# Kernel optimization log

Measured on AMD Instinct MI355X. Metric: run time of the kernel, lower is better.

The kernel has to match this reference:

```python
import jax, jax.numpy as jnp
import numpy as np

B, L, H, NH, NB = 8, 200, 128, 4, 2
HD = H // NH
ITEM_NUM, TIME_SPAN = 50000, 256
PAD = -2.0**32 + 1.0


def setup_inputs() -> dict:
    key = jax.random.key(0)
    ks = jax.random.split(key, 32)
    def g(i, shape, s=0.02):
        return jax.random.normal(ks[i], shape, jnp.float32) * s
    item_emb = g(0, (ITEM_NUM + 1, H)).at[0].set(0.0)  # padding_idx=0
    return dict(
        user_ids=jax.random.randint(ks[1], (B,), 0, 1000),
        log_seqs=jax.random.randint(ks[2], (B, L), 0, ITEM_NUM),
        time_matrices=jax.random.randint(ks[3], (B, L, L), 0, TIME_SPAN + 1),
        pos_seqs=jax.random.randint(ks[4], (B, L), 0, ITEM_NUM + 1),
        neg_seqs=jax.random.randint(ks[5], (B, L), 0, ITEM_NUM + 1),
        item_emb=item_emb,
        pos_K_emb=g(6, (L, H)), pos_V_emb=g(7, (L, H)),
        time_K_emb=g(8, (TIME_SPAN + 1, H)), time_V_emb=g(9, (TIME_SPAN + 1, H)),
        attn_ln_g=jnp.ones((NB, H)), attn_ln_b=jnp.zeros((NB, H)),
        Wq=g(10, (NB, H, H)), bq=jnp.zeros((NB, H)),
        Wk=g(11, (NB, H, H)), bk=jnp.zeros((NB, H)),
        Wv=g(12, (NB, H, H)), bv=jnp.zeros((NB, H)),
        fwd_ln_g=jnp.ones((NB, H)), fwd_ln_b=jnp.zeros((NB, H)),
        W1=g(13, (NB, H, H)), b1=jnp.zeros((NB, H)),
        W2=g(14, (NB, H, H)), b2=jnp.zeros((NB, H)),
        last_ln_g=jnp.ones((H,)), last_ln_b=jnp.zeros((H,)),
    )


def _ln(x, g, b, eps=1e-8):
    m = x.mean(-1, keepdims=True)
    v = jnp.var(x, axis=-1, keepdims=True)
    return (x - m) / jnp.sqrt(v + eps) * g + b


def _heads(x):
    # [..., H] -> [NH, ..., HD]; matches torch.cat(torch.split(x, HD, -1), 0)
    y = x.reshape(x.shape[:-1] + (NH, HD))
    return jnp.moveaxis(y, -2, 0)


def reference(user_ids, log_seqs, time_matrices, pos_seqs, neg_seqs, item_emb,
              pos_K_emb, pos_V_emb, time_K_emb, time_V_emb,
              attn_ln_g, attn_ln_b, Wq, bq, Wk, bk, Wv, bv,
              fwd_ln_g, fwd_ln_b, W1, b1, W2, b2, last_ln_g, last_ln_b):
    # user_ids is unused in the original forward as well.
    tmask = log_seqs == 0                                  # [B,L] True = pad
    keep = (~tmask)[..., None].astype(jnp.float32)
    seqs = item_emb[log_seqs] * np.float32(np.sqrt(H))
    seqs = seqs * keep
    pKh = _heads(pos_K_emb)                                # [NH,L,HD]
    pVh = _heads(pos_V_emb)
    tKh = _heads(time_K_emb[time_matrices])                # [NH,B,L,L,HD]
    tVh = _heads(time_V_emb[time_matrices])
    causal = ~jnp.tril(jnp.ones((L, L), bool))             # True above diag -> masked
    bad = tmask[:, :, None] | causal[None]                 # [B,L,L]
    scale = np.float32(np.sqrt(HD))
    for i in range(NB):
        Qin = _ln(seqs, attn_ln_g[i], attn_ln_b[i])
        Qh = _heads(Qin @ Wq[i].T + bq[i])                 # [NH,B,L,HD]
        Kh = _heads(seqs @ Wk[i].T + bk[i])
        Vh = _heads(seqs @ Wv[i].T + bv[i])
        attn = (jnp.einsum('nbqd,nbkd->nbqk', Qh, Kh)
                + jnp.einsum('nbqd,nkd->nbqk', Qh, pKh)
                + jnp.einsum('nbqkd,nbqd->nbqk', tKh, Qh)) / scale
        attn = jnp.where(bad[None], PAD, attn)
        attn = jax.nn.softmax(attn, axis=-1)
        out = (jnp.einsum('nbqk,nbkd->nbqd', attn, Vh)
               + jnp.einsum('nbqk,nkd->nbqd', attn, pVh)
               + jnp.einsum('nbqk,nbqkd->nbqd', attn, tVh))
        out = jnp.moveaxis(out, 0, -2).reshape(seqs.shape)  # merge heads -> [B,L,H]
        seqs = Qin + out                                    # residual uses LN'd Q (as in source)
        seqs = _ln(seqs, fwd_ln_g[i], fwd_ln_b[i])
        ff = jax.nn.relu(seqs @ W1[i].T + b1[i]) @ W2[i].T + b2[i] + seqs
        seqs = ff * keep
    log_feats = _ln(seqs, last_ln_g, last_ln_b)
    pos_logits = (log_feats * item_emb[pos_seqs]).sum(-1)   # [B,L]
    neg_logits = (log_feats * item_emb[neg_seqs]).sum(-1)
    return pos_logits, neg_logits
```

## Files before the change

### kernel.cpp

```cpp
#include <hip/hip_runtime.h>

#define BB 8
#define LL 200
#define HH 128
#define NHEAD 4
#define HDIM 32
#define NBLK 2
#define BL (BB * LL)
#define NT 257
#define QT 8
#define NQT 25
#define SSP 208
#define KTP 66
#define TSP 132

static constexpr float SQRT_H    = 11.313708498984761f;
static constexpr float INV_SCALE = 0.17677669529663687f;
static constexpr float PADV      = -4294967295.0f;

__global__ void k_qkv_gemm(const float* __restrict__ seqs_in,
                           const int* __restrict__ log_seqs,
                           const float* __restrict__ item_emb,
                           const float* __restrict__ g, const float* __restrict__ bia,
                           const float* __restrict__ Wq, const float* __restrict__ bq,
                           const float* __restrict__ Wk, const float* __restrict__ bk,
                           const float* __restrict__ Wv, const float* __restrict__ bv,
                           const float* __restrict__ posK, const float* __restrict__ posV,
                           float* __restrict__ Qin, float* __restrict__ Q,
                           float* __restrict__ K, float* __restrict__ V) {
    int mt = blockIdx.x / 24, nt = blockIdx.x % 24;
    int matsel = nt >> 3;
    int jb = (nt & 7) * 16;
    int row0 = mt * 32;
    int tid = threadIdx.x;
    __shared__ float As[32 * TSP];
    __shared__ float Bs[16 * TSP];

    {
        int r = tid >> 3, seg = tid & 7;
        int row = row0 + r;
        float4 vv[4];
        if (seqs_in) {
            #pragma unroll
            for (int i = 0; i < 4; i++)
                vv[i] = *(const float4*)(seqs_in + (size_t)row * HH + seg * 16 + i * 4);
        } else {
            int idx = log_seqs[row];
            if (idx == 0) {
                #pragma unroll
                for (int i = 0; i < 4; i++) vv[i] = make_float4(0.f, 0.f, 0.f, 0.f);
            } else {
                #pragma unroll
                for (int i = 0; i < 4; i++) {
                    float4 e = *(const float4*)(item_emb + (size_t)idx * HH + seg * 16 + i * 4);
                    vv[i] = make_float4(e.x * SQRT_H, e.y * SQRT_H, e.z * SQRT_H, e.w * SQRT_H);
                }
            }
        }
        if (matsel == 0) {
            float s = 0.f, s2 = 0.f;
            #pragma unroll
            for (int i = 0; i < 4; i++) {
                s  += vv[i].x + vv[i].y + vv[i].z + vv[i].w;
                s2 += vv[i].x * vv[i].x + vv[i].y * vv[i].y + vv[i].z * vv[i].z + vv[i].w * vv[i].w;
            }
            #pragma unroll
            for (int off = 1; off < 8; off <<= 1) {
                s  += __shfl_xor(s, off);
                s2 += __shfl_xor(s2, off);
            }
            float mean = s * (1.f / HH);
            float var  = s2 * (1.f / HH) - mean * mean;
            float inv  = 1.f / sqrtf(var + 1e-8f);
            #pragma unroll
            for (int i = 0; i < 4; i++) {
                int k = seg * 16 + i * 4;
                float4 g4 = *(const float4*)(g + k);
                float4 b4 = *(const float4*)(bia + k);
                float4 y;
                y.x = (vv[i].x - mean) * inv * g4.x + b4.x;
                y.y = (vv[i].y - mean) * inv * g4.y + b4.y;
                y.z = (vv[i].z - mean) * inv * g4.z + b4.z;
                y.w = (vv[i].w - mean) * inv * g4.w + b4.w;
                *(float4*)&As[r * TSP + k] = y;
                if (nt == 0) *(float4*)(Qin + (size_t)row * HH + k) = y;
            }
        } else {
            #pragma unroll
            for (int i = 0; i < 4; i++)
                *(float4*)&As[r * TSP + seg * 16 + i * 4] = vv[i];
        }
    }
    {
        const float* W = (matsel == 0) ? Wq : (matsel == 1) ? Wk : Wv;
        int j = tid >> 4, seg = tid & 15;
        float4 w  = *(const float4*)(W + (size_t)(jb + j) * HH + seg * 8);
        float4 w2 = *(const float4*)(W + (size_t)(jb + j) * HH + seg * 8 + 4);
        *(float4*)&Bs[j * TSP + seg * 8]     = w;
        *(float4*)&Bs[j * TSP + seg * 8 + 4] = w2;
    }
    __syncthreads();

    int m = tid >> 3, jg = tid & 7;
    float acc0 = 0.f, acc1 = 0.f;
    const float* ar  = &As[m * TSP];
    const float* b0r = &Bs[(jg * 2) * TSP];
    const float* b1r = &Bs[(jg * 2 + 1) * TSP];
    #pragma unroll 4
    for (int k4 = 0; k4 < 32; k4++) {
        float4 a  = *(const float4*)(ar + k4 * 4);
        float4 b0 = *(const float4*)(b0r + k4 * 4);
        float4 b1 = *(const float4*)(b1r + k4 * 4);
        acc0 += a.x * b0.x + a.y * b0.y + a.z * b0.z + a.w * b0.w;
        acc1 += a.x * b1.x + a.y * b1.y + a.z * b1.z + a.w * b1.w;
    }
    int row = row0 + m;
    int col = jb + jg * 2;
    int l = row % LL;
    if (matsel == 0) {
        float2 bb = *(const float2*)(bq + col);
        *(float2*)(Q + (size_t)row * HH + col) =
            make_float2((acc0 + bb.x) * INV_SCALE, (acc1 + bb.y) * INV_SCALE);
    } else if (matsel == 1) {
        float2 bb = *(const float2*)(bk + col);
        float2 pk = *(const float2*)(posK + (size_t)l * HH + col);
        *(float2*)(K + (size_t)row * HH + col) =
            make_float2(acc0 + bb.x + pk.x, acc1 + bb.y + pk.y);
    } else {
        float2 bb = *(const float2*)(bv + col);
        float2 pv = *(const float2*)(posV + (size_t)l * HH + col);
        *(float2*)(V + (size_t)row * HH + col) =
            make_float2(acc0 + bb.x + pv.x, acc1 + bb.y + pv.y);
    }
}

__global__ void k_attn(const float* __restrict__ Q, const float* __restrict__ K,
                       const float* __restrict__ V,
                       const float* __restrict__ timeK, const float* __restrict__ timeV,
                       const int* __restrict__ tm,
                       float* __restrict__ att) {
    int bn = blockIdx.x & 31;
    int b = bn >> 2, n = bn & 3;
    int qt = (NQT - 1) - (blockIdx.x >> 5);
    int q0 = qt * QT;
    int kmax = q0 + QT - 1;
    int tid = threadIdx.x;
    int wv = tid >> 6, ln = tid & 63;

    __shared__ float KstT[2][HDIM * KTP];
    __shared__ float DTW[QT * NT];
    __shared__ float Ssc[QT * SSP];
    __shared__ float Ost[QT * HDIM];
    __shared__ int   tmst[QT * LL];

    Ost[tid] = 0.f;
    #pragma unroll
    for (int qi = 0; qi < QT; qi++)
        if (tid < LL)
            tmst[qi * LL + tid] = tm[((size_t)(b * LL + q0 + qi)) * LL + tid];

    int k2 = tid & 31, qi_c = tid >> 5;
    int q = q0 + qi_c;

    float qreg[HDIM];
    {
        const float* qp = Q + ((size_t)(b * LL + q)) * HH + n * HDIM;
        #pragma unroll
        for (int i = 0; i < 8; i++) {
            float4 v = *(const float4*)(qp + i * 4);
            qreg[i * 4 + 0] = v.x; qreg[i * 4 + 1] = v.y;
            qreg[i * 4 + 2] = v.z; qreg[i * 4 + 3] = v.w;
        }
    }

    const int nchS = (kmax >> 6) + 1;
    const int ncht = 5 + nchS;

    auto stage = [&](int c, float* buf) {
        #pragma unroll
        for (int p = 0; p < 2; p++) {
            int idx = tid + p * 256;
            int r = idx >> 3, d4 = idx & 7;
            float4 w = make_float4(0.f, 0.f, 0.f, 0.f);
            if (c < 5) {
                int tau = c * 64 + r;
                if (tau < NT) w = *(const float4*)(timeK + (size_t)tau * HH + n * HDIM + d4 * 4);
            } else {
                int k = (c - 5) * 64 + r;
                if (k < LL) w = *(const float4*)(K + ((size_t)(b * LL + k)) * HH + n * HDIM + d4 * 4);
            }
            buf[(d4 * 4 + 0) * KTP + r] = w.x;
            buf[(d4 * 4 + 1) * KTP + r] = w.y;
            buf[(d4 * 4 + 2) * KTP + r] = w.z;
            buf[(d4 * 4 + 3) * KTP + r] = w.w;
        }
    };

    stage(0, KstT[0]);
    __syncthreads();
    for (int c = 0; c < ncht; c++) {
        if (c + 1 < ncht) stage(c + 1, KstT[(c + 1) & 1]);
        const float* buf = KstT[c & 1];
        float a0 = 0.f, a1 = 0.f;
        #pragma unroll 4
        for (int d = 0; d < HDIM; d++) {
            float qv = qreg[d];
            float2 kv = *(const float2*)&buf[d * KTP + k2 * 2];
            a0 += qv * kv.x; a1 += qv * kv.y;
        }
        if (c < 5) {
            int tau0 = c * 64 + k2 * 2;
            if (tau0 < NT)     DTW[qi_c * NT + tau0]     = a0;
            if (tau0 + 1 < NT) DTW[qi_c * NT + tau0 + 1] = a1;
        } else {
            int k0 = (c - 5) * 64 + k2 * 2;
            if (k0 <= kmax)     Ssc[qi_c * SSP + k0]     = a0;
            if (k0 + 1 <= kmax) Ssc[qi_c * SSP + k0 + 1] = a1;
        }
        __syncthreads();
    }

    for (int rr = 0; rr < 2; rr++) {
        int qi = wv + rr * 4;
        int qq = q0 + qi;
        float sv[4];
        float m = PADV;
        #pragma unroll
        for (int jj = 0; jj < 4; jj++) {
            int k = ln + 64 * jj;
            sv[jj] = (k <= qq) ? (Ssc[qi * SSP + k] + DTW[qi * NT + tmst[qi * LL + k]]) : PADV;
            m = fmaxf(m, sv[jj]);
        }
        for (int off = 32; off; off >>= 1) m = fmaxf(m, __shfl_xor(m, off));
        float sum = 0.f;
        #pragma unroll
        for (int jj = 0; jj < 4; jj++) {
            int k = ln + 64 * jj;
            sv[jj] = (k <= qq) ? __expf(sv[jj] - m) : 0.f;
            sum += sv[jj];
        }
        for (int off = 32; off; off >>= 1) sum += __shfl_xor(sum, off);
        float inv = 1.f / sum;
        #pragma unroll
        for (int jj = 0; jj < 4; jj++) {
            int k = ln + 64 * jj;
            if (k < SSP) Ssc[qi * SSP + k] = (k <= qq) ? sv[jj] * inv : 0.f;
        }
    }
    __syncthreads();

    int d = tid & 31, kg = tid >> 5;
    float acc[QT] = {0,0,0,0,0,0,0,0};
    const float* vb  = V + ((size_t)(b * LL)) * HH + n * HDIM + d;
    const float* tvb = timeV + n * HDIM + d;
    for (int k = kg; k <= kmax; k += 8) {
        float v = vb[(size_t)k * HH];
        #pragma unroll
        for (int qi = 0; qi < QT; qi++) {
            float p  = Ssc[qi * SSP + k];
            float tv = tvb[(size_t)tmst[qi * LL + k] * HH];
            acc[qi] += p * (v + tv);
        }
    }
    #pragma unroll
    for (int qi = 0; qi < QT; qi++) atomicAdd(&Ost[qi * HDIM + d], acc[qi]);
    __syncthreads();
    {
        int qi = tid >> 5;
        att[((size_t)(b * LL + q0 + qi)) * HH + n * HDIM + (tid & 31)] = Ost[tid];
    }
}

__global__ void k_ff1(const float* __restrict__ Qin, const float* __restrict__ att,
                      const float* __restrict__ g, const float* __restrict__ bia,
                      const float* __restrict__ W1, const float* __restrict__ b1,
                      float* __restrict__ h1) {
    int mt = blockIdx.x >> 3, jb = (blockIdx.x & 7) * 16;
    int row0 = mt * 16;
    int tid = threadIdx.x;
    __shared__ float As[16 * TSP];
    __shared__ float Bs[16 * TSP];

    {
        int r = tid >> 4, seg = tid & 15;
        int row = row0 + r;
        float4 vv[2];
        #pragma unroll
        for (int i = 0; i < 2; i++) {
            int k = seg * 8 + i * 4;
            float4 q4 = *(const float4*)(Qin + (size_t)row * HH + k);
            float4 a4 = *(const float4*)(att + (size_t)row * HH + k);
            vv[i] = make_float4(q4.x + a4.x, q4.y + a4.y, q4.z + a4.z, q4.w + a4.w);
        }
        float s = 0.f, s2 = 0.f;
        #pragma unroll
        for (int i = 0; i < 2; i++) {
            s  += vv[i].x + vv[i].y + vv[i].z + vv[i].w;
            s2 += vv[i].x * vv[i].x + vv[i].y * vv[i].y + vv[i].z * vv[i].z + vv[i].w * vv[i].w;
        }
        #pragma unroll
        for (int off = 1; off < 16; off <<= 1) {
            s  += __shfl_xor(s, off);
            s2 += __shfl_xor(s2, off);
        }
        float mean = s * (1.f / HH);
        float var  = s2 * (1.f / HH) - mean * mean;
        float inv  = 1.f / sqrtf(var + 1e-8f);
        #pragma unroll
        for (int i = 0; i < 2; i++) {
            int k = seg * 8 + i * 4;
            float4 g4 = *(const float4*)(g + k);
            float4 b4 = *(const float4*)(bia + k);
            float4 y;
            y.x = (vv[i].x - mean) * inv * g4.x + b4.x;
            y.y = (vv[i].y - mean) * inv * g4.y + b4.y;
            y.z = (vv[i].z - mean) * inv * g4.z + b4.z;
            y.w = (vv[i].w - mean) * inv * g4.w + b4.w;
            *(float4*)&As[r * TSP + k] = y;
        }
    }
    {
        int j = tid >> 4, seg = tid & 15;
        *(float4*)&Bs[j * TSP + seg * 8]     = *(const float4*)(W1 + (size_t)(jb + j) * HH + seg * 8);
        *(float4*)&Bs[j * TSP + seg * 8 + 4] = *(const float4*)(W1 + (size_t)(jb + j) * HH + seg * 8 + 4);
    }
    __syncthreads();

    int m = tid >> 4, j = tid & 15;
    float acc = 0.f;
    const float* ar = &As[m * TSP];
    const float* br = &Bs[j * TSP];
    #pragma unroll 4
    for (int k4 = 0; k4 < 32; k4++) {
        float4 a = *(const float4*)(ar + k4 * 4);
        float4 b = *(const float4*)(br + k4 * 4);
        acc += a.x * b.x + a.y * b.y + a.z * b.z + a.w * b.w;
    }
    int col = jb + j;
    float t = acc + b1[col];
    h1[(size_t)(row0 + m) * HH + col] = t > 0.f ? t : 0.f;
}

__global__ void k_ff2(const float* __restrict__ h1,
                      const float* __restrict__ Qin, const float* __restrict__ att,
                      const float* __restrict__ g, const float* __restrict__ bia,
                      const float* __restrict__ W2, const float* __restrict__ b2,
                      const int* __restrict__ log_seqs,
                      float* __restrict__ out) {
    int mt = blockIdx.x >> 3, jb = (blockIdx.x & 7) * 16;
    int row0 = mt * 16;
    int tid = threadIdx.x;
    __shared__ float As[16 * TSP];
    __shared__ float Bs[16 * TSP];
    __shared__ float mu[16], rstd[16];

    {
        int r = tid >> 4, seg = tid & 15;
        int row = row0 + r;
        #pragma unroll
        for (int i = 0; i < 2; i++) {
            int k = seg * 8 + i * 4;
            *(float4*)&As[r * TSP + k] = *(const float4*)(h1 + (size_t)row * HH + k);
        }
        float s = 0.f, s2 = 0.f;
        #pragma unroll
        for (int i = 0; i < 2; i++) {
            int k = seg * 8 + i * 4;
            float4 q4 = *(const float4*)(Qin + (size_t)row * HH + k);
            float4 a4 = *(const float4*)(att + (size_t)row * HH + k);
            float4 v = make_float4(q4.x + a4.x, q4.y + a4.y, q4.z + a4.z, q4.w + a4.w);
            s  += v.x + v.y + v.z + v.w;
            s2 += v.x * v.x + v.y * v.y + v.z * v.z + v.w * v.w;
        }
        #pragma unroll
        for (int off = 1; off < 16; off <<= 1) {
            s  += __shfl_xor(s, off);
            s2 += __shfl_xor(s2, off);
        }
        float mean = s * (1.f / HH);
        float var  = s2 * (1.f / HH) - mean * mean;
        if (seg == 0) { mu[r] = mean; rstd[r] = 1.f / sqrtf(var + 1e-8f); }
    }
    {
        int j = tid >> 4, seg = tid & 15;
        *(float4*)&Bs[j * TSP + seg * 8]     = *(const float4*)(W2 + (size_t)(jb + j) * HH + seg * 8);
        *(float4*)&Bs[j * TSP + seg * 8 + 4] = *(const float4*)(W2 + (size_t)(jb + j) * HH + seg * 8 + 4);
    }
    __syncthreads();

    int m = tid >> 4, j = tid & 15;
    float acc = 0.f;
    const float* ar = &As[m * TSP];
    const float* br = &Bs[j * TSP];
    #pragma unroll 4
    for (int k4 = 0; k4 < 32; k4++) {
        float4 a = *(const float4*)(ar + k4 * 4);
        float4 b = *(const float4*)(br + k4 * 4);
        acc += a.x * b.x + a.y * b.y + a.z * b.z + a.w * b.w;
    }
    int row = row0 + m;
    int col = jb + j;
    float resid = Qin[(size_t)row * HH + col] + att[(size_t)row * HH + col];
    float y = (resid - mu[m]) * rstd[m] * g[col] + bia[col];
    float o = acc + b2[col] + y;
    if (log_seqs[row] == 0) o = 0.f;
    out[(size_t)row * HH + col] = o;
}

__global__ void k_lnlogits(const float* __restrict__ seqs,
                           const float* __restrict__ g, const float* __restrict__ bia,
                           const float* __restrict__ item_emb,
                           const int* __restrict__ pos, const int* __restrict__ neg,
                           float* __restrict__ out) {
    int row = blockIdx.x;
    int h = threadIdx.x;
    float v = seqs[(size_t)row * HH + h];
    float s = v, s2 = v * v;
    for (int off = 32; off; off >>= 1) {
        s  += __shfl_xor(s, off);
        s2 += __shfl_xor(s2, off);
    }
    __shared__ float r1[2], r2[2];
    if ((h & 63) == 0) { r1[h >> 6] = s; r2[h >> 6] = s2; }
    __syncthreads();
    float mean = (r1[0] + r1[1]) * (1.f / HH);
    float var  = (r2[0] + r2[1]) * (1.f / HH) - mean * mean;
    float inv = 1.f / sqrtf(var + 1e-8f);
    float f = (v - mean) * inv * g[h] + bia[h];

    int ip = pos[row], in_ = neg[row];
    float vp = f * item_emb[(size_t)ip * HH + h];
    float vn = f * item_emb[(size_t)in_ * HH + h];
    for (int off = 32; off; off >>= 1) {
        vp += __shfl_xor(vp, off);
        vn += __shfl_xor(vn, off);
    }
    __shared__ float rp[2], rn[2];
    if ((h & 63) == 0) { rp[h >> 6] = vp; rn[h >> 6] = vn; }
    __syncthreads();
    if (h == 0) {
        out[row]      = rp[0] + rp[1];
        out[BL + row] = rn[0] + rn[1];
    }
}

extern "C" void kernel_launch(void* const* d_in, const int* in_sizes, int n_in,
                              void* d_out, int out_size, void* d_ws, size_t ws_size,
                              hipStream_t stream) {
    const int* log_seqs   = (const int*)d_in[1];
    const int* tm         = (const int*)d_in[2];
    const int* pos_seqs   = (const int*)d_in[3];
    const int* neg_seqs   = (const int*)d_in[4];
    const float* item_emb = (const float*)d_in[5];
    const float* posK     = (const float*)d_in[6];
    const float* posV     = (const float*)d_in[7];
    const float* timeK    = (const float*)d_in[8];
    const float* timeV    = (const float*)d_in[9];
    const float* attn_g   = (const float*)d_in[10];
    const float* attn_b   = (const float*)d_in[11];
    const float* Wq       = (const float*)d_in[12];
    const float* bq       = (const float*)d_in[13];
    const float* Wk       = (const float*)d_in[14];
    const float* bk       = (const float*)d_in[15];
    const float* Wv       = (const float*)d_in[16];
    const float* bv       = (const float*)d_in[17];
    const float* fwd_g    = (const float*)d_in[18];
    const float* fwd_b    = (const float*)d_in[19];
    const float* W1       = (const float*)d_in[20];
    const float* b1       = (const float*)d_in[21];
    const float* W2       = (const float*)d_in[22];
    const float* b2       = (const float*)d_in[23];
    const float* last_g   = (const float*)d_in[24];
    const float* last_b   = (const float*)d_in[25];

    float* seqs = (float*)d_ws;
    float* Qin  = seqs + (size_t)BL * HH;
    float* Qb   = Qin  + (size_t)BL * HH;
    float* Kb   = Qb   + (size_t)BL * HH;
    float* Vb   = Kb   + (size_t)BL * HH;
    float* att  = Vb   + (size_t)BL * HH;
    float* h1   = att  + (size_t)BL * HH;

    for (int i = 0; i < NBLK; i++) {
        k_qkv_gemm<<<1200, 256, 0, stream>>>(i == 0 ? nullptr : seqs, log_seqs, item_emb,
                                             attn_g + i * HH, attn_b + i * HH,
                                             Wq + (size_t)i * HH * HH, bq + i * HH,
                                             Wk + (size_t)i * HH * HH, bk + i * HH,
                                             Wv + (size_t)i * HH * HH, bv + i * HH,
                                             posK, posV, Qin, Qb, Kb, Vb);
        k_attn<<<NQT * 32, 256, 0, stream>>>(Qb, Kb, Vb, timeK, timeV, tm, att);
        k_ff1<<<800, 256, 0, stream>>>(Qin, att, fwd_g + i * HH, fwd_b + i * HH,
                                       W1 + (size_t)i * HH * HH, b1 + i * HH, h1);
        k_ff2<<<800, 256, 0, stream>>>(h1, Qin, att, fwd_g + i * HH, fwd_b + i * HH,
                                       W2 + (size_t)i * HH * HH, b2 + i * HH,
                                       log_seqs, seqs);
    }
    k_lnlogits<<<BL, HH, 0, stream>>>(seqs, last_g, last_b, item_emb,
                                      pos_seqs, neg_seqs, (float*)d_out);
}
```

Baseline: 236.4 us.

## Reuse A tiles across four column tiles in GEMMs and register-prefetch attention staging

The QKV, FF1 and FF2 GEMM kernels now have each block loop over four 16-column weight tiles with double-buffered shared memory. The normalized A tile is loaded once per four output tiles instead of once per tile, which cuts grid sizes by 4x and removes redundant LayerNorm and activation loads. The attention kernel splits K/timeK staging into a register load issued before the compute loop and a shared-memory write after it, so global latency overlaps compute. In exchange, grids become small (200–300 blocks on a many-CU part), which lowers parallelism, and each GEMM block adds more __syncthreads.

After: 235.1 us. No clear change (-0.5%).

```diff
diff --git a/kernel.cpp b/kernel.cpp
--- a/kernel.cpp
+++ b/kernel.cpp
@@ -28,13 +28,14 @@
                            const float* __restrict__ posK, const float* __restrict__ posV,
                            float* __restrict__ Qin, float* __restrict__ Q,
                            float* __restrict__ K, float* __restrict__ V) {
-    int mt = blockIdx.x / 24, nt = blockIdx.x % 24;
-    int matsel = nt >> 3;
-    int jb = (nt & 7) * 16;
+    int mt = blockIdx.x / 6, ntg = blockIdx.x % 6;
+    int nt0 = ntg * 4;
+    int matsel = nt0 >> 3;
+    int jb0 = (nt0 & 7) * 16;
     int row0 = mt * 32;
     int tid = threadIdx.x;
     __shared__ float As[32 * TSP];
-    __shared__ float Bs[16 * TSP];
+    __shared__ float Bs[2][16 * TSP];
 
     {
         int r = tid >> 3, seg = tid & 7;
@@ -83,7 +84,7 @@
                 y.z = (vv[i].z - mean) * inv * g4.z + b4.z;
                 y.w = (vv[i].w - mean) * inv * g4.w + b4.w;
                 *(float4*)&As[r * TSP + k] = y;
-                if (nt == 0) *(float4*)(Qin + (size_t)row * HH + k) = y;
+                if (nt0 == 0) *(float4*)(Qin + (size_t)row * HH + k) = y;
             }
         } else {
             #pragma unroll
@@ -91,46 +92,58 @@
                 *(float4*)&As[r * TSP + seg * 16 + i * 4] = vv[i];
         }
     }
-    {
-        const float* W = (matsel == 0) ? Wq : (matsel == 1) ? Wk : Wv;
-        int j = tid >> 4, seg = tid & 15;
-        float4 w  = *(const float4*)(W + (size_t)(jb + j) * HH + seg * 8);
-        float4 w2 = *(const float4*)(W + (size_t)(jb + j) * HH + seg * 8 + 4);
-        *(float4*)&Bs[j * TSP + seg * 8]     = w;
-        *(float4*)&Bs[j * TSP + seg * 8 + 4] = w2;
-    }
+    const float* W = (matsel == 0) ? Wq : (matsel == 1) ? Wk : Wv;
+    int j = tid >> 4, seg16 = tid & 15;
+    float4 w0 = *(const float4*)(W + (size_t)(jb0 + j) * HH + seg16 * 8);
+    float4 w1 = *(const float4*)(W + (size_t)(jb0 + j) * HH + seg16 * 8 + 4);
+    *(float4*)&Bs[0][j * TSP + seg16 * 8]     = w0;
+    *(float4*)&Bs[0][j * TSP + seg16 * 8 + 4] = w1;
     __syncthreads();
 
     int m = tid >> 3, jg = tid & 7;
-    float acc0 = 0.f, acc1 = 0.f;
-    const float* ar  = &As[m * TSP];
-    const float* b0r = &Bs[(jg * 2) * TSP];
-    const float* b1r = &Bs[(jg * 2 + 1) * TSP];
-    #pragma unroll 4
-    for (int k4 = 0; k4 < 32; k4++) {
-        float4 a  = *(const float4*)(ar + k4 * 4);
-        float4 b0 = *(const float4*)(b0r + k4 * 4);
-        float4 b1 = *(const float4*)(b1r + k4 * 4);
-        acc0 += a.x * b0.x + a.y * b0.y + a.z * b0.z + a.w * b0.w;
-        acc1 += a.x * b1.x + a.y * b1.y + a.z * b1.z + a.w * b1.w;
-    }
-    int row = row0 + m;
-    int col = jb + jg * 2;
-    int l = row % LL;
-    if (matsel == 0) {
-        float2 bb = *(const float2*)(bq + col);
-        *(float2*)(Q + (size_t)row * HH + col) =
-            make_float2((acc0 + bb.x) * INV_SCALE, (acc1 + bb.y) * INV_SCALE);
-    } else if (matsel == 1) {
-        float2 bb = *(const float2*)(bk + col);
-        float2 pk = *(const float2*)(posK + (size_t)l * HH + col);
-        *(float2*)(K + (size_t)row * HH + col) =
-            make_float2(acc0 + bb.x + pk.x, acc1 + bb.y + pk.y);
-    } else {
-        float2 bb = *(const float2*)(bv + col);
-        float2 pv = *(const float2*)(posV + (size_t)l * HH + col);
-        *(float2*)(V + (size_t)row * HH + col) =
-            make_float2(acc0 + bb.x + pv.x, acc1 + bb.y + pv.y);
+    const float* ar = &As[m * TSP];
+    #pragma unroll
+    for (int it = 0; it < 4; it++) {
+        int jb = jb0 + it * 16;
+        if (it < 3) {
+            int jbn = jb0 + (it + 1) * 16;
+            w0 = *(const float4*)(W + (size_t)(jbn + j) * HH + seg16 * 8);
+            w1 = *(const float4*)(W + (size_t)(jbn + j) * HH + seg16 * 8 + 4);
+        }
+        float acc0 = 0.f, acc1 = 0.f;
+        const float* b0r = &Bs[it & 1][(jg * 2) * TSP];
+        const float* b1r = &Bs[it & 1][(jg * 2 + 1) * TSP];
+        #pragma unroll 4
+        for (int k4 = 0; k4 < 32; k4++) {
+            float4 a  = *(const float4*)(ar + k4 * 4);
+            float4 b0 = *(const float4*)(b0r + k4 * 4);
+            float4 b1 = *(const float4*)(b1r + k4 * 4);
+            acc0 += a.x * b0.x + a.y * b0.y + a.z * b0.z + a.w * b0.w;
+            acc1 += a.x * b1.x + a.y * b1.y + a.z * b1.z + a.w * b1.w;
+        }
+        int row = row0 + m;
+        int col = jb + jg * 2;
+        int l = row % LL;
+        if (matsel == 0) {
+            float2 bb = *(const float2*)(bq + col);
+            *(float2*)(Q + (size_t)row * HH + col) =
+                make_float2((acc0 + bb.x) * INV_SCALE, (acc1 + bb.y) * INV_SCALE);
+        } else if (matsel == 1) {
+            float2 bb = *(const float2*)(bk + col);
+            float2 pk = *(const float2*)(posK + (size_t)l * HH + col);
+            *(float2*)(K + (size_t)row * HH + col) =
+                make_float2(acc0 + bb.x + pk.x, acc1 + bb.y + pk.y);
+        } else {
+            float2 bb = *(const float2*)(bv + col);
+            float2 pv = *(const float2*)(posV + (size_t)l * HH + col);
+            *(float2*)(V + (size_t)row * HH + col) =
+                make_float2(acc0 + bb.x + pv.x, acc1 + bb.y + pv.y);
+        }
+        if (it < 3) {
+            *(float4*)&Bs[(it + 1) & 1][j * TSP + seg16 * 8]     = w0;
+            *(float4*)&Bs[(it + 1) & 1][j * TSP + seg16 * 8 + 4] = w1;
+        }
+        __syncthreads();
     }
 }
 
@@ -176,30 +189,42 @@
     const int nchS = (kmax >> 6) + 1;
     const int ncht = 5 + nchS;
 
-    auto stage = [&](int c, float* buf) {
-        #pragma unroll
-        for (int p = 0; p < 2; p++) {
-            int idx = tid + p * 256;
-            int r = idx >> 3, d4 = idx & 7;
-            float4 w = make_float4(0.f, 0.f, 0.f, 0.f);
-            if (c < 5) {
-                int tau = c * 64 + r;
-                if (tau < NT) w = *(const float4*)(timeK + (size_t)tau * HH + n * HDIM + d4 * 4);
-            } else {
-                int k = (c - 5) * 64 + r;
-                if (k < LL) w = *(const float4*)(K + ((size_t)(b * LL + k)) * HH + n * HDIM + d4 * 4);
-            }
-            buf[(d4 * 4 + 0) * KTP + r] = w.x;
-            buf[(d4 * 4 + 1) * KTP + r] = w.y;
-            buf[(d4 * 4 + 2) * KTP + r] = w.z;
-            buf[(d4 * 4 + 3) * KTP + r] = w.w;
+    int rS = tid >> 3, d4 = tid & 7;
+
+    auto ld_chunk = [&](int c, float4& f0, float4& f1) {
+        f0 = make_float4(0.f, 0.f, 0.f, 0.f);
+        f1 = make_float4(0.f, 0.f, 0.f, 0.f);
+        if (c < 5) {
+            int tau = c * 64 + rS;
+            if (tau < NT)      f0 = *(const float4*)(timeK + (size_t)tau * HH + n * HDIM + d4 * 4);
+            if (tau + 32 < NT) f1 = *(const float4*)(timeK + (size_t)(tau + 32) * HH + n * HDIM + d4 * 4);
+        } else {
+            int k = (c - 5) * 64 + rS;
+            if (k < LL)      f0 = *(const float4*)(K + ((size_t)(b * LL + k)) * HH + n * HDIM + d4 * 4);
+            if (k + 32 < LL) f1 = *(const float4*)(K + ((size_t)(b * LL + k + 32)) * HH + n * HDIM + d4 * 4);
         }
     };
-
-    stage(0, KstT[0]);
+    auto wr_chunk = [&](float4 f0, float4 f1, float* buf) {
+        buf[(d4 * 4 + 0) * KTP + rS] = f0.x;
+        buf[(d4 * 4 + 1) * KTP + rS] = f0.y;
+        buf[(d4 * 4 + 2) * KTP + rS] = f0.z;
+        buf[(d4 * 4 + 3) * KTP + rS] = f0.w;
+        buf[(d4 * 4 + 0) * KTP + rS + 32] = f1.x;
+        buf[(d4 * 4 + 1) * KTP + rS + 32] = f1.y;
+        buf[(d4 * 4 + 2) * KTP + rS + 32] = f1.z;
+        buf[(d4 * 4 + 3) * KTP + rS + 32] = f1.w;
+    };
+
+    {
+        float4 c0, c1;
+        ld_chunk(0, c0, c1);
+        wr_chunk(c0, c1, KstT[0]);
+    }
     __syncthreads();
     for (int c = 0; c < ncht; c++) {
-        if (c + 1 < ncht) stage(c + 1, KstT[(c + 1) & 1]);
+        float4 n0, n1;
+        bool more = (c + 1 < ncht);
+        if (more) ld_chunk(c + 1, n0, n1);
         const float* buf = KstT[c & 1];
         float a0 = 0.f, a1 = 0.f;
         #pragma unroll 4
@@ -217,6 +242,7 @@
             if (k0 <= kmax)     Ssc[qi_c * SSP + k0]     = a0;
             if (k0 + 1 <= kmax) Ssc[qi_c * SSP + k0 + 1] = a1;
         }
+        if (more) wr_chunk(n0, n1, KstT[(c + 1) & 1]);
         __syncthreads();
     }
 
@@ -275,11 +301,11 @@
                       const float* __restrict__ g, const float* __restrict__ bia,
                       const float* __restrict__ W1, const float* __restrict__ b1,
                       float* __restrict__ h1) {
-    int mt = blockIdx.x >> 3, jb = (blockIdx.x & 7) * 16;
+    int mt = blockIdx.x >> 1, jb0 = (blockIdx.x & 1) * 64;
     int row0 = mt * 16;
     int tid = threadIdx.x;
     __shared__ float As[16 * TSP];
-    __shared__ float Bs[16 * TSP];
+    __shared__ float Bs[2][16 * TSP];
 
     {
         int r = tid >> 4, seg = tid & 15;
@@ -319,26 +345,40 @@
             *(float4*)&As[r * TSP + k] = y;
         }
     }
-    {
-        int j = tid >> 4, seg = tid & 15;
-        *(float4*)&Bs[j * TSP + seg * 8]     = *(const float4*)(W1 + (size_t)(jb + j) * HH + seg * 8);
-        *(float4*)&Bs[j * TSP + seg * 8 + 4] = *(const float4*)(W1 + (size_t)(jb + j) * HH + seg * 8 + 4);
-    }
-    __syncthreads();
-
-    int m = tid >> 4, j = tid & 15;
-    float acc = 0.f;
+    int j = tid >> 4, seg16 = tid & 15;
+    float4 w0 = *(const float4*)(W1 + (size_t)(jb0 + j) * HH + seg16 * 8);
+    float4 w1 = *(const float4*)(W1 + (size_t)(jb0 + j) * HH + seg16 * 8 + 4);
+    *(float4*)&Bs[0][j * TSP + seg16 * 8]     = w0;
+    *(float4*)&Bs[0][j * TSP + seg16 * 8 + 4] = w1;
+    __syncthreads();
+
+    int m = tid >> 4, jj = tid & 15;
     const float* ar = &As[m * TSP];
-    const float* br = &Bs[j * TSP];
-    #pragma unroll 4
-    for (int k4 = 0; k4 < 32; k4++) {
-        float4 a = *(const float4*)(ar + k4 * 4);
-        float4 b = *(const float4*)(br + k4 * 4);
-        acc += a.x * b.x + a.y * b.y + a.z * b.z + a.w * b.w;
-    }
-    int col = jb + j;
-    float t = acc + b1[col];
-    h1[(size_t)(row0 + m) * HH + col] = t > 0.f ? t : 0.f;
+    #pragma unroll
+    for (int it = 0; it < 4; it++) {
+        int jb = jb0 + it * 16;
+        if (it < 3) {
+            int jbn = jb0 + (it + 1) * 16;
+            w0 = *(const float4*)(W1 + (size_t)(jbn + j) * HH + seg16 * 8);
+            w1 = *(const float4*)(W1 + (size_t)(jbn + j) * HH + seg16 * 8 + 4);
+        }
+        float acc = 0.f;
+        const float* br = &Bs[it & 1][jj * TSP];
+        #pragma unroll 4
+        for (int k4 = 0; k4 < 32; k4++) {
+            float4 a = *(const float4*)(ar + k4 * 4);
+            float4 b = *(const float4*)(br + k4 * 4);
+            acc += a.x * b.x + a.y * b.y + a.z * b.z + a.w * b.w;
+        }
+        int col = jb + jj;
+        float t = acc + b1[col];
+        h1[(size_t)(row0 + m) * HH + col] = t > 0.f ? t : 0.f;
+        if (it < 3) {
+            *(float4*)&Bs[(it + 1) & 1][j * TSP + seg16 * 8]     = w0;
+            *(float4*)&Bs[(it + 1) & 1][j * TSP + seg16 * 8 + 4] = w1;
+        }
+        __syncthreads();
+    }
 }
 
 __global__ void k_ff2(const float* __restrict__ h1,
@@ -347,11 +387,11 @@
                       const float* __restrict__ W2, const float* __restrict__ b2,
                       const int* __restrict__ log_seqs,
                       float* __restrict__ out) {
-    int mt = blockIdx.x >> 3, jb = (blockIdx.x & 7) * 16;
+    int mt = blockIdx.x >> 1, jb0 = (blockIdx.x & 1) * 64;
     int row0 = mt * 16;
     int tid = threadIdx.x;
     __shared__ float As[16 * TSP];
-    __shared__ float Bs[16 * TSP];
+    __shared__ float Bs[2][16 * TSP];
     __shared__ float mu[16], rstd[16];
 
     {
@@ -381,30 +421,44 @@
         float var  = s2 * (1.f / HH) - mean * mean;
         if (seg == 0) { mu[r] = mean; rstd[r] = 1.f / sqrtf(var + 1e-8f); }
     }
-    {
-        int j = tid >> 4, seg = tid & 15;
-        *(float4*)&Bs[j * TSP + seg * 8]     = *(const float4*)(W2 + (size_t)(jb + j) * HH + seg * 8);
-        *(float4*)&Bs[j * TSP + seg * 8 + 4] = *(const float4*)(W2 + (size_t)(jb + j) * HH + seg * 8 + 4);
-    }
-    __syncthreads();
-
-    int m = tid >> 4, j = tid & 15;
-    float acc = 0.f;
+    int j = tid >> 4, seg16 = tid & 15;
+    float4 w0 = *(const float4*)(W2 + (size_t)(jb0 + j) * HH + seg16 * 8);
+    float4 w1 = *(const float4*)(W2 + (size_t)(jb0 + j) * HH + seg16 * 8 + 4);
+    *(float4*)&Bs[0][j * TSP + seg16 * 8]     = w0;
+    *(float4*)&Bs[0][j * TSP + seg16 * 8 + 4] = w1;
+    __syncthreads();
+
+    int m = tid >> 4, jj = tid & 15;
     const float* ar = &As[m * TSP];
-    const float* br = &Bs[j * TSP];
-    #pragma unroll 4
-    for (int k4 = 0; k4 < 32; k4++) {
-        float4 a = *(const float4*)(ar + k4 * 4);
-        float4 b = *(const float4*)(br + k4 * 4);
-        acc += a.x * b.x + a.y * b.y + a.z * b.z + a.w * b.w;
-    }
-    int row = row0 + m;
-    int col = jb + j;
-    float resid = Qin[(size_t)row * HH + col] + att[(size_t)row * HH + col];
-    float y = (resid - mu[m]) * rstd[m] * g[col] + bia[col];
-    float o = acc + b2[col] + y;
-    if (log_seqs[row] == 0) o = 0.f;
-    out[(size_t)row * HH + col] = o;
+    #pragma unroll
+    for (int it = 0; it < 4; it++) {
+        int jb = jb0 + it * 16;
+        if (it < 3) {
+            int jbn = jb0 + (it + 1) * 16;
+            w0 = *(const float4*)(W2 + (size_t)(jbn + j) * HH + seg16 * 8);
+            w1 = *(const float4*)(W2 + (size_t)(jbn + j) * HH + seg16 * 8 + 4);
+        }
+        float acc = 0.f;
+        const float* br = &Bs[it & 1][jj * TSP];
+        #pragma unroll 4
+        for (int k4 = 0; k4 < 32; k4++) {
+            float4 a = *(const float4*)(ar + k4 * 4);
+            float4 b = *(const float4*)(br + k4 * 4);
+            acc += a.x * b.x + a.y * b.y + a.z * b.z + a.w * b.w;
+        }
+        int row = row0 + m;
+        int col = jb + jj;
+        float resid = Qin[(size_t)row * HH + col] + att[(size_t)row * HH + col];
+        float y = (resid - mu[m]) * rstd[m] * g[col] + bia[col];
+        float o = acc + b2[col] + y;
+        if (log_seqs[row] == 0) o = 0.f;
+        out[(size_t)row * HH + col] = o;
+        if (it < 3) {
+            *(float4*)&Bs[(it + 1) & 1][j * TSP + seg16 * 8]     = w0;
+            *(float4*)&Bs[(it + 1) & 1][j * TSP + seg16 * 8 + 4] = w1;
+        }
+        __syncthreads();
+    }
 }
 
 __global__ void k_lnlogits(const float* __restrict__ seqs,
@@ -482,16 +536,16 @@
     float* h1   = att  + (size_t)BL * HH;
 
     for (int i = 0; i < NBLK; i++) {
-        k_qkv_gemm<<<1200, 256, 0, stream>>>(i == 0 ? nullptr : seqs, log_seqs, item_emb,
-                                             attn_g + i * HH, attn_b + i * HH,
-                                             Wq + (size_t)i * HH * HH, bq + i * HH,
-                                             Wk + (size_t)i * HH * HH, bk + i * HH,
-                                             Wv + (size_t)i * HH * HH, bv + i * HH,
-                                             posK, posV, Qin, Qb, Kb, Vb);
+        k_qkv_gemm<<<300, 256, 0, stream>>>(i == 0 ? nullptr : seqs, log_seqs, item_emb,
+                                            attn_g + i * HH, attn_b + i * HH,
+                                            Wq + (size_t)i * HH * HH, bq + i * HH,
+                                            Wk + (size_t)i * HH * HH, bk + i * HH,
+                                            Wv + (size_t)i * HH * HH, bv + i * HH,
+                                            posK, posV, Qin, Qb, Kb, Vb);
         k_attn<<<NQT * 32, 256, 0, stream>>>(Qb, Kb, Vb, timeK, timeV, tm, att);
-        k_ff1<<<800, 256, 0, stream>>>(Qin, att, fwd_g + i * HH, fwd_b + i * HH,
+        k_ff1<<<200, 256, 0, stream>>>(Qin, att, fwd_g + i * HH, fwd_b + i * HH,
                                        W1 + (size_t)i * HH * HH, b1 + i * HH, h1);
-        k_ff2<<<800, 256, 0, stream>>>(h1, Qin, att, fwd_g + i * HH, fwd_b + i * HH,
+        k_ff2<<<200, 256, 0, stream>>>(h1, Qin, att, fwd_g + i * HH, fwd_b + i * HH,
                                        W2 + (size_t)i * HH * HH, b2 + i * HH,
                                        log_seqs, seqs);
     }
```
